# Kernel tuning notes

Hardware: AMD Instinct MI355X
Metric: run time of the kernel (lower is better)

The kernel has to match this reference:

```python
import jax, jax.numpy as jnp
import numpy as np

N_DRUG, D, K = 846, 64, 1024
N_REL, N_ENT = 200, 100000
BN_EPS = 1e-5

def setup_inputs() -> dict:
    key = jax.random.key(0)
    ks = jax.random.split(key, 10)
    return {
        "drug_table": jax.random.normal(ks[0], (N_DRUG, D), jnp.float32),
        "rela_table": jax.random.normal(ks[1], (N_REL, D), jnp.float32),
        "ent_table": jax.random.normal(ks[2], (N_ENT, D), jnp.float32),
        "W1": jax.random.normal(ks[3], (N_DRUG, D, D), jnp.float32),
        "b1": jax.random.normal(ks[4], (K, D), jnp.float32),
        "W2": jax.random.normal(ks[5], (N_DRUG, D, D), jnp.float32),
        "b2": jax.random.normal(ks[6], (K, D), jnp.float32),
        "lin_w": jax.random.normal(ks[7], (D, 2 * D), jnp.float32) * (6.0 / (3 * D)) ** 0.5,
        "lin_b": jnp.zeros((D,), jnp.float32),
        "bn_w": jnp.ones((D,), jnp.float32),
        "bn_b": jnp.zeros((D,), jnp.float32),
        "drug_name": jnp.arange(N_DRUG, dtype=jnp.int64 if jax.config.jax_enable_x64 else jnp.int32),
        "adj_tail": jax.random.randint(ks[8], (N_DRUG, K), 0, N_ENT),
        "adj_relation": jax.random.randint(ks[9], (N_DRUG, K), 0, N_REL),
    }

def reference(drug_table, rela_table, ent_table, W1, b1, W2, b2,
              lin_w, lin_b, bn_w, bn_b, drug_name, adj_tail, adj_relation):
    drug_emb = drug_table[drug_name]          # [N, D]
    rela_emb = rela_table[adj_relation]       # [N, K, D]
    ent_emb = ent_table[adj_tail]             # [N, K, D]
    # per-drug relation-modulated transform
    drug_rel = drug_emb[:, None, :] * rela_emb                     # [N, K, D]
    h = jax.nn.relu(jnp.einsum('nkd,nde->nke', drug_rel, W1) + b1)  # [N, K, D]
    h = jnp.einsum('nkd,nde->nke', h, W2) + b2                      # [N, K, D]
    score = jax.nn.softmax(jnp.sum(h, axis=-1), axis=1)             # [N, K]
    weighted_ent = jnp.einsum('nk,nkd->nd', score, ent_emb)         # [N, D]
    drug_e = jnp.concatenate([weighted_ent, drug_emb], axis=1)      # [N, 2D]
    y = jax.nn.relu(drug_e @ lin_w.T + lin_b)                       # [N, D]
    # BatchNorm1d in training mode: biased batch statistics
    mean = jnp.mean(y, axis=0)
    var = jnp.mean((y - mean) ** 2, axis=0)
    out = (y - mean) * jax.lax.rsqrt(var + BN_EPS) * bn_w + bn_b
    return out
```

## Files before the change

kernel.cpp:

```cpp
#include <hip/hip_runtime.h>


#define NDRUG 846
#define KNB   1024
#define NREL  200
#define BN_EPS 1e-5f

#define NW2   ((NDRUG*64 + 255)/256)
#define NRELT 13312
#define NRELB (NRELT/256)

typedef __attribute__((ext_vector_type(8))) short short8;
typedef __attribute__((ext_vector_type(4))) float f32x4;

__device__ __forceinline__ unsigned short f2bf(float x){
    unsigned u = __float_as_uint(x);
    unsigned r = u + 0x7fffu + ((u >> 16) & 1u);
    return (unsigned short)(r >> 16);
}
__device__ __forceinline__ float bf2f(unsigned short h){
    return __uint_as_float(((unsigned)h) << 16);
}

__global__ void prep_kernel(const float* __restrict__ b2, const float* __restrict__ W2,
                            const float* __restrict__ rela_table,
                            float* __restrict__ b2s, float* __restrict__ w2sum_g,
                            unsigned short* __restrict__ relah,
                            unsigned short* __restrict__ relal){
    int b = blockIdx.x;
    int t = threadIdx.x;
    if (b < 4){
        int k = b*256 + t;
        const float4* p = (const float4*)(b2 + (size_t)k*64);
        float s = 0.f;
        #pragma unroll
        for (int i = 0; i < 16; ++i){ float4 v = p[i]; s += v.x+v.y+v.z+v.w; }
        b2s[k] = s;
    } else if (b < 4 + NW2){
        int idx = (b - 4)*256 + t;
        if (idx < NDRUG*64){
            const float4* p = (const float4*)(W2 + (size_t)idx*64);
            float s = 0.f;
            #pragma unroll
            for (int i = 0; i < 16; ++i){ float4 v = p[i]; s += v.x+v.y+v.z+v.w; }
            w2sum_g[idx] = s;
        }
    } else {
        int idx = (b - 4 - NW2)*256 + t;
        int j  = idx & 7;
        int ln = (idx >> 3) & 63;
        int ss = (idx >> 9) & 1;
        int mt = idx >> 10;
        int r = mt*16 + (ln & 15); if (r > 199) r = 199;
        int d = ss*32 + ((ln >> 4) << 3) + j;
        float v = rela_table[r*64 + d];
        unsigned short h = (unsigned short)(__float_as_uint(v) >> 16);
        relah[idx] = h;
        relal[idx] = f2bf(v - bf2f(h));
    }
}

__global__ __launch_bounds__(512) void gnn_a4x(
    const float* __restrict__ drug_table, const unsigned short* __restrict__ relah,
    const unsigned short* __restrict__ relal,
    const float* __restrict__ W1,         const float* __restrict__ b1,
    const float* __restrict__ w2sum_g,    const int* __restrict__ drug_name,
    const int* __restrict__ adj_rel,
    float* __restrict__ scoresA,          float* __restrict__ scoresB)
{
    __shared__ __align__(16) float sS[6400];
    __shared__ __align__(16) float w2s[32];
    __shared__ float drug[64];
    unsigned short* Bh = (unsigned short*)sS;
    unsigned short* Bl = (unsigned short*)(sS + 1024);

    const int t = threadIdx.x;
    const int lane = t & 63;
    const int w = t >> 6;
    const int lg = lane >> 4;
    const int l15 = lane & 15;
    const int n = blockIdx.x;
    const int ehalf = blockIdx.y;
    const int e_base = ehalf << 5;

    if (t < 64) drug[t] = drug_table[(size_t)drug_name[n]*64 + t];
    if (t >= 64 && t < 96) w2s[t - 64] = w2sum_g[n*64 + e_base + (t - 64)];
    __syncthreads();

    {
        const float* W1n = W1 + (size_t)n*4096;
        #pragma unroll
        for (int p = 0; p < 4; ++p){
            int idx = p*512 + t;
            int d = idx >> 5, eo = idx & 31;
            float v = W1n[d*64 + e_base + eo] * drug[d];
            int ss = d >> 5, j = d & 7, lgb = (d >> 3) & 3, nn = eo >> 4;
            int ln = (lgb << 4) | (eo & 15);
            int dst = (((ss<<1)|nn)*64 + ln)*8 + j;
            unsigned short h = (unsigned short)(__float_as_uint(v) >> 16);
            Bh[dst] = h;
            Bl[dst] = f2bf(v - bf2f(h));
        }
    }
    __syncthreads();

    short8 bhr[4], blr[4];
    #pragma unroll
    for (int f = 0; f < 4; ++f){
        bhr[f] = *(const short8*)&Bh[(f*64 + lane)*8];
        blr[f] = *(const short8*)&Bl[(f*64 + lane)*8];
    }
    __syncthreads();

    const short8* Ah_t = (const short8*)relah;
    const short8* Al_t = (const short8*)relal;

    #pragma unroll 1
    for (int mi = 0; mi < 2; ++mi){
        int mt = w + 8*mi;
        if (mt < 13){
            short8 Ah0 = Ah_t[(mt*2+0)*64 + lane];
            short8 Ah1 = Ah_t[(mt*2+1)*64 + lane];
            short8 Al0 = Al_t[(mt*2+0)*64 + lane];
            short8 Al1 = Al_t[(mt*2+1)*64 + lane];
            f32x4 acc[2] = {};
            #pragma unroll
            for (int nn = 0; nn < 2; ++nn){
                acc[nn] = __builtin_amdgcn_mfma_f32_16x16x32_bf16(Ah0, bhr[nn],   acc[nn], 0,0,0);
                acc[nn] = __builtin_amdgcn_mfma_f32_16x16x32_bf16(Ah0, blr[nn],   acc[nn], 0,0,0);
                acc[nn] = __builtin_amdgcn_mfma_f32_16x16x32_bf16(Al0, bhr[nn],   acc[nn], 0,0,0);
                acc[nn] = __builtin_amdgcn_mfma_f32_16x16x32_bf16(Ah1, bhr[2+nn], acc[nn], 0,0,0);
                acc[nn] = __builtin_amdgcn_mfma_f32_16x16x32_bf16(Ah1, blr[2+nn], acc[nn], 0,0,0);
                acc[nn] = __builtin_amdgcn_mfma_f32_16x16x32_bf16(Al1, bhr[2+nn], acc[nn], 0,0,0);
            }
            int rb = mt*16 + (lg<<2);
            #pragma unroll
            for (int nn = 0; nn < 2; ++nn){
                int eo = (nn<<4) | l15;
                int slot = eo >> 2, wrd = eo & 3;
                #pragma unroll
                for (int q = 0; q < 4; ++q){
                    int r = rb + q;
                    if (r < 200)
                        sS[r*32 + ((slot ^ (r & 7))<<2) + wrd] = acc[nn][q];
                }
            }
        }
    }
    __syncthreads();

    const int* arel = adj_rel + (size_t)n*KNB;
    float* sout = (ehalf ? scoresB : scoresA) + (size_t)n*KNB;
    const int ec = lane & 3;
    f32x4 w2r[2];
    #pragma unroll
    for (int j = 0; j < 2; ++j) w2r[j] = *(const f32x4*)&w2s[ec*8 + j*4];

    int rr8[8];
    #pragma unroll
    for (int pass = 0; pass < 8; ++pass)
        rr8[pass] = arel[pass*128 + w*16 + (lane >> 2)];

    #pragma unroll 2
    for (int pass = 0; pass < 8; ++pass){
        int k = pass*128 + w*16 + (lane >> 2);
        int rr = rr8[pass];
        const float* b1p = b1 + (size_t)k*64 + e_base + ec*8;
        float sc = 0.f;
        #pragma unroll
        for (int j = 0; j < 2; ++j){
            int slot = ec*2 + j;
            f32x4 s4 = *(const f32x4*)&sS[rr*32 + ((slot ^ (rr & 7))<<2)];
            f32x4 bq = *(const f32x4*)(b1p + 4*j);
            #pragma unroll
            for (int q = 0; q < 4; ++q)
                sc += fmaxf(s4[q] + bq[q], 0.f) * w2r[j][q];
        }
        sc += __shfl_xor(sc, 1);
        sc += __shfl_xor(sc, 2);
        if (ec == 0) sout[k] = sc;
    }
}

__global__ __launch_bounds__(256,6) void softgather(
    const float* __restrict__ scoresA,  const float* __restrict__ scoresB,
    const float* __restrict__ b2s,
    const int* __restrict__ adj_tail,   const float* __restrict__ ent_table,
    const float* __restrict__ drug_table, const int* __restrict__ drug_name,
    const float* __restrict__ lin_w,    const float* __restrict__ lin_b,
    float* __restrict__ y_out)
{
    __shared__ float sE[KNB];
    __shared__ int list[KNB];
    __shared__ int segc[17];
    __shared__ float red[256];
    __shared__ float wepart[4][64];
    __shared__ float de[128];

    const int t = threadIdx.x;
    const int lane = t & 63;
    const int w = t >> 6;
    const int n = blockIdx.x;

    float dpre = 0.f;
    if (t < 64) dpre = drug_table[(size_t)drug_name[n]*64 + t];

    const float* sgA = scoresA + (size_t)n*KNB;
    const float* sgB = scoresB + (size_t)n*KNB;
    float sv[4]; float mx = -1e30f;
    #pragma unroll
    for (int i = 0; i < 4; ++i){
        int k = t + (i<<8);
        sv[i] = sgA[k] + sgB[k] + b2s[k];
        mx = fmaxf(mx, sv[i]);
    }
    #pragma unroll
    for (int off = 1; off < 64; off <<= 1) mx = fmaxf(mx, __shfl_xor(mx, off, 64));
    if (lane == 0) red[w] = mx;
    __syncthreads();
    mx = fmaxf(fmaxf(red[0], red[1]), fmaxf(red[2], red[3]));
    float ei[4]; float ps = 0.f;
    #pragma unroll
    for (int i = 0; i < 4; ++i){
        ei[i] = __expf(sv[i] - mx);
        sE[t + (i<<8)] = ei[i];
        ps += ei[i];
    }
    #pragma unroll
    for (int off = 1; off < 64; off <<= 1) ps += __shfl_xor(ps, off, 64);
    if (lane == 0) red[8 + w] = ps;
    __syncthreads();
    const float inv = 1.f / (red[8]+red[9]+red[10]+red[11]);

    unsigned long long bal[4]; int pos[4];
    #pragma unroll
    for (int i = 0; i < 4; ++i){
        bool nz = (ei[i] != 0.f);
        bal[i] = __ballot(nz);
        pos[i] = (int)__popcll(bal[i] & ((1ull << lane) - 1ull));
        if (lane == 0) segc[i*4 + w] = (int)__popcll(bal[i]);
    }
    __syncthreads();
    if (t == 0){
        int acc = 0;
        #pragma unroll
        for (int s = 0; s < 16; ++s){ int c = segc[s]; segc[s] = acc; acc += c; }
        segc[16] = acc;
    }
    __syncthreads();
    #pragma unroll
    for (int i = 0; i < 4; ++i){
        if (ei[i] != 0.f)
            list[segc[i*4 + w] + pos[i]] = (i<<8) + (w<<6) + lane;
    }
    const int C = segc[16];
    __syncthreads();

    const int* atail = adj_tail + (size_t)n*KNB;
    float awe = 0.f;
    {
        int j = w;
        float ev0 = 0.f, row0 = 0.f;
        if (j < C){
            int k0 = list[j];
            ev0 = sE[k0];
            row0 = ent_table[(size_t)atail[k0]*64 + lane];
        }
        while (j < C){
            int jn = j + 4;
            float ev1 = 0.f, row1 = 0.f;
            if (jn < C){
                int k1 = list[jn];
                ev1 = sE[k1];
                row1 = ent_table[(size_t)atail[k1]*64 + lane];
            }
            awe += ev0 * row0;
            ev0 = ev1; row0 = row1; j = jn;
        }
    }
    wepart[w][lane] = awe;
    __syncthreads();
    if (t < 64){
        de[t]    = (wepart[0][t]+wepart[1][t]+wepart[2][t]+wepart[3][t]) * inv;
        de[64+t] = dpre;
    }
    __syncthreads();

    float yp = 0.f;
    #pragma unroll
    for (int ii = 0; ii < 32; ++ii){
        int i = w*32 + ii;
        yp += de[i] * lin_w[lane*128 + i];
    }
    red[t] = yp;
    __syncthreads();
    if (t < 64){
        float yv = lin_b[t] + red[t] + red[64+t] + red[128+t] + red[192+t];
        y_out[(size_t)n*64 + t] = fmaxf(yv, 0.f);
    }
}

__global__ void bn_kernel(const float* __restrict__ y, const float* __restrict__ bn_w,
                          const float* __restrict__ bn_b, float* __restrict__ out){
    __shared__ float r1[4], r2[4];
    const int j = blockIdx.x;
    const int t = threadIdx.x;
    float s1 = 0.f, s2 = 0.f;
    for (int i = t; i < NDRUG; i += 256){
        float v = y[(size_t)i*64 + j];
        s1 += v; s2 += v*v;
    }
    #pragma unroll
    for (int off = 1; off < 64; off <<= 1){
        s1 += __shfl_xor(s1, off, 64);
        s2 += __shfl_xor(s2, off, 64);
    }
    int w = t >> 6, lane = t & 63;
    if (lane == 0){ r1[w] = s1; r2[w] = s2; }
    __syncthreads();
    s1 = r1[0]+r1[1]+r1[2]+r1[3];
    s2 = r2[0]+r2[1]+r2[2]+r2[3];
    float mean = s1 * (1.f/NDRUG);
    float var  = s2 * (1.f/NDRUG) - mean*mean;
    float sc = rsqrtf(var + BN_EPS) * bn_w[j];
    float sh = bn_b[j] - mean*sc;
    for (int i = t; i < NDRUG; i += 256)
        out[(size_t)i*64 + j] = y[(size_t)i*64 + j]*sc + sh;
}

extern "C" void kernel_launch(void* const* d_in, const int* in_sizes, int n_in,
                              void* d_out, int out_size, void* d_ws, size_t ws_size,
                              hipStream_t stream) {
    const float* drug_table = (const float*)d_in[0];
    const float* rela_table = (const float*)d_in[1];
    const float* ent_table  = (const float*)d_in[2];
    const float* W1    = (const float*)d_in[3];
    const float* b1    = (const float*)d_in[4];
    const float* W2    = (const float*)d_in[5];
    const float* b2    = (const float*)d_in[6];
    const float* lin_w = (const float*)d_in[7];
    const float* lin_b = (const float*)d_in[8];
    const float* bn_w  = (const float*)d_in[9];
    const float* bn_b  = (const float*)d_in[10];
    const int* drug_name = (const int*)d_in[11];
    const int* adj_tail  = (const int*)d_in[12];
    const int* adj_rel   = (const int*)d_in[13];
    float* out = (float*)d_out;

    float* b2s     = (float*)d_ws;
    float* yb      = b2s + KNB;
    float* w2sumg  = yb + NDRUG*64;
    float* scoresA = w2sumg + NDRUG*64;
    float* scoresB = scoresA + (size_t)NDRUG*KNB;
    unsigned short* relah = (unsigned short*)(scoresB + (size_t)NDRUG*KNB);
    unsigned short* relal = relah + NRELT;

    prep_kernel<<<4 + NW2 + NRELB, 256, 0, stream>>>(
        b2, W2, rela_table, b2s, w2sumg, relah, relal);
    gnn_a4x<<<dim3(NDRUG,2), 512, 0, stream>>>(drug_table, relah, relal, W1, b1,
                                               w2sumg, drug_name, adj_rel,
                                               scoresA, scoresB);
    softgather<<<NDRUG, 256, 0, stream>>>(scoresA, scoresB, b2s, adj_tail, ent_table,
                                          drug_table, drug_name, lin_w, lin_b, yb);
    bn_kernel<<<64, 256, 0, stream>>>(yb, bn_w, bn_b, out);
}
```

Baseline: 47.29 us.

## Precompute drug-scaled split-bf16 W1 fragments in prep kernel

Moves the drug-scaled W1 conversion into bf16 hi/lo MFMA-fragment layout out of the main scoring kernel and into the prep kernel, which now writes it to workspace. The scoring kernel loads B fragments straight from global memory, dropping its shared-memory staging and two block barriers. W1 is read once per drug instead of once per e-half, but this adds a global write and re-read of the converted fragments and a larger, LDS-heavy prep kernel.

```diff
diff --git a/kernel.cpp b/kernel.cpp
--- a/kernel.cpp
+++ b/kernel.cpp
@@ -9,6 +9,7 @@
 #define NW2   ((NDRUG*64 + 255)/256)
 #define NRELT 13312
 #define NRELB (NRELT/256)
+#define PREPW1 (4 + NW2 + NRELB)
 
 typedef __attribute__((ext_vector_type(8))) short short8;
 typedef __attribute__((ext_vector_type(4))) float f32x4;
@@ -24,9 +25,16 @@
 
 __global__ void prep_kernel(const float* __restrict__ b2, const float* __restrict__ W2,
                             const float* __restrict__ rela_table,
+                            const float* __restrict__ drug_table,
+                            const float* __restrict__ W1,
+                            const int* __restrict__ drug_name,
                             float* __restrict__ b2s, float* __restrict__ w2sum_g,
                             unsigned short* __restrict__ relah,
-                            unsigned short* __restrict__ relal){
+                            unsigned short* __restrict__ relal,
+                            unsigned short* __restrict__ w1h,
+                            unsigned short* __restrict__ w1l){
+    __shared__ float drugs[64];
+    __shared__ unsigned short BhL[4096], BlL[4096];
     int b = blockIdx.x;
     int t = threadIdx.x;
     if (b < 4){
@@ -45,7 +53,7 @@
             for (int i = 0; i < 16; ++i){ float4 v = p[i]; s += v.x+v.y+v.z+v.w; }
             w2sum_g[idx] = s;
         }
-    } else {
+    } else if (b < PREPW1){
         int idx = (b - 4 - NW2)*256 + t;
         int j  = idx & 7;
         int ln = (idx >> 3) & 63;
@@ -57,22 +65,46 @@
         unsigned short h = (unsigned short)(__float_as_uint(v) >> 16);
         relah[idx] = h;
         relal[idx] = f2bf(v - bf2f(h));
-    }
-}
-
-__global__ __launch_bounds__(512) void gnn_a4x(
-    const float* __restrict__ drug_table, const unsigned short* __restrict__ relah,
-    const unsigned short* __restrict__ relal,
-    const float* __restrict__ W1,         const float* __restrict__ b1,
-    const float* __restrict__ w2sum_g,    const int* __restrict__ drug_name,
+    } else {
+        int n = b - PREPW1;
+        if (t < 64) drugs[t] = drug_table[(size_t)drug_name[n]*64 + t];
+        __syncthreads();
+        const float* W1n = W1 + (size_t)n*4096;
+        #pragma unroll
+        for (int p = 0; p < 16; ++p){
+            int idx = p*256 + t;
+            int d = idx >> 6, e = idx & 63;
+            float v = W1n[idx] * drugs[d];
+            int ss = d >> 5, j = d & 7, lgb = (d >> 3) & 3;
+            int f = ss*4 + (e >> 4);
+            int ln = (lgb << 4) | (e & 15);
+            int dst = (f*64 + ln)*8 + j;
+            unsigned short h = (unsigned short)(__float_as_uint(v) >> 16);
+            BhL[dst] = h;
+            BlL[dst] = f2bf(v - bf2f(h));
+        }
+        __syncthreads();
+        short8* outh = (short8*)w1h + (size_t)n*512;
+        short8* outl = (short8*)w1l + (size_t)n*512;
+        const short8* inh = (const short8*)BhL;
+        const short8* inl = (const short8*)BlL;
+        #pragma unroll
+        for (int it = 0; it < 2; ++it){
+            outh[it*256 + t] = inh[it*256 + t];
+            outl[it*256 + t] = inl[it*256 + t];
+        }
+    }
+}
+
+__global__ __launch_bounds__(512) void gnn_b(
+    const unsigned short* __restrict__ relah, const unsigned short* __restrict__ relal,
+    const unsigned short* __restrict__ w1h,   const unsigned short* __restrict__ w1l,
+    const float* __restrict__ b1,             const float* __restrict__ w2sum_g,
     const int* __restrict__ adj_rel,
-    float* __restrict__ scoresA,          float* __restrict__ scoresB)
+    float* __restrict__ scoresA,              float* __restrict__ scoresB)
 {
     __shared__ __align__(16) float sS[6400];
     __shared__ __align__(16) float w2s[32];
-    __shared__ float drug[64];
-    unsigned short* Bh = (unsigned short*)sS;
-    unsigned short* Bl = (unsigned short*)(sS + 1024);
 
     const int t = threadIdx.x;
     const int lane = t & 63;
@@ -83,34 +115,19 @@
     const int ehalf = blockIdx.y;
     const int e_base = ehalf << 5;
 
-    if (t < 64) drug[t] = drug_table[(size_t)drug_name[n]*64 + t];
-    if (t >= 64 && t < 96) w2s[t - 64] = w2sum_g[n*64 + e_base + (t - 64)];
-    __syncthreads();
-
-    {
-        const float* W1n = W1 + (size_t)n*4096;
-        #pragma unroll
-        for (int p = 0; p < 4; ++p){
-            int idx = p*512 + t;
-            int d = idx >> 5, eo = idx & 31;
-            float v = W1n[d*64 + e_base + eo] * drug[d];
-            int ss = d >> 5, j = d & 7, lgb = (d >> 3) & 3, nn = eo >> 4;
-            int ln = (lgb << 4) | (eo & 15);
-            int dst = (((ss<<1)|nn)*64 + ln)*8 + j;
-            unsigned short h = (unsigned short)(__float_as_uint(v) >> 16);
-            Bh[dst] = h;
-            Bl[dst] = f2bf(v - bf2f(h));
-        }
-    }
-    __syncthreads();
-
+    if (t < 32) w2s[t] = w2sum_g[n*64 + e_base + t];
+
+    const short8* bht = (const short8*)w1h + (size_t)n*512;
+    const short8* blt = (const short8*)w1l + (size_t)n*512;
     short8 bhr[4], blr[4];
     #pragma unroll
-    for (int f = 0; f < 4; ++f){
-        bhr[f] = *(const short8*)&Bh[(f*64 + lane)*8];
-        blr[f] = *(const short8*)&Bl[(f*64 + lane)*8];
-    }
-    __syncthreads();
+    for (int ss = 0; ss < 2; ++ss)
+        #pragma unroll
+        for (int nn = 0; nn < 2; ++nn){
+            int f = ss*4 + ehalf*2 + nn;
+            bhr[ss*2+nn] = bht[f*64 + lane];
+            blr[ss*2+nn] = blt[f*64 + lane];
+        }
 
     const short8* Ah_t = (const short8*)relah;
     const short8* Al_t = (const short8*)relal;
@@ -354,12 +371,14 @@
     float* scoresB = scoresA + (size_t)NDRUG*KNB;
     unsigned short* relah = (unsigned short*)(scoresB + (size_t)NDRUG*KNB);
     unsigned short* relal = relah + NRELT;
-
-    prep_kernel<<<4 + NW2 + NRELB, 256, 0, stream>>>(
-        b2, W2, rela_table, b2s, w2sumg, relah, relal);
-    gnn_a4x<<<dim3(NDRUG,2), 512, 0, stream>>>(drug_table, relah, relal, W1, b1,
-                                               w2sumg, drug_name, adj_rel,
-                                               scoresA, scoresB);
+    unsigned short* w1h   = relal + NRELT;
+    unsigned short* w1l   = w1h + (size_t)NDRUG*4096;
+
+    prep_kernel<<<PREPW1 + NDRUG, 256, 0, stream>>>(
+        b2, W2, rela_table, drug_table, W1, drug_name,
+        b2s, w2sumg, relah, relal, w1h, w1l);
+    gnn_b<<<dim3(NDRUG,2), 512, 0, stream>>>(relah, relal, w1h, w1l, b1,
+                                             w2sumg, adj_rel, scoresA, scoresB);
     softgather<<<NDRUG, 256, 0, stream>>>(scoresA, scoresB, b2s, adj_tail, ent_table,
                                           drug_table, drug_name, lin_w, lin_b, yb);
     bn_kernel<<<64, 256, 0, stream>>>(yb, bn_w, bn_b, out);
```

Result: slower. 51.10 us (+8.1%).

## Fuse score kernel and softmax-gather kernel into one per-drug block

Applied to the files above, without the earlier changes.

Merges the two-half score computation and the softmax/gather/linear kernel into a single 512-thread block per drug. Each block now loops over both 32-column halves itself, keeping the scores in shared memory instead of writing them to global and reading them back. This removes the global score round-trip and one kernel launch. In exchange the grid shrinks from 2x846 blocks to 846, with more shared memory per block, which reduces parallelism and occupancy.

```diff
diff --git a/kernel.cpp b/kernel.cpp
--- a/kernel.cpp
+++ b/kernel.cpp
@@ -60,19 +60,29 @@
     }
 }
 
-__global__ __launch_bounds__(512) void gnn_a4x(
+__global__ __launch_bounds__(512) void fused_drug(
     const float* __restrict__ drug_table, const unsigned short* __restrict__ relah,
     const unsigned short* __restrict__ relal,
     const float* __restrict__ W1,         const float* __restrict__ b1,
-    const float* __restrict__ w2sum_g,    const int* __restrict__ drug_name,
-    const int* __restrict__ adj_rel,
-    float* __restrict__ scoresA,          float* __restrict__ scoresB)
+    const float* __restrict__ w2sum_g,    const float* __restrict__ b2s,
+    const int* __restrict__ drug_name,    const int* __restrict__ adj_rel,
+    const int* __restrict__ adj_tail,     const float* __restrict__ ent_table,
+    const float* __restrict__ lin_w,      const float* __restrict__ lin_b,
+    float* __restrict__ y_out)
 {
     __shared__ __align__(16) float sS[6400];
-    __shared__ __align__(16) float w2s[32];
+    __shared__ __align__(16) unsigned short Bbuf[8192];
+    __shared__ __align__(16) float w2s[64];
     __shared__ float drug[64];
-    unsigned short* Bh = (unsigned short*)sS;
-    unsigned short* Bl = (unsigned short*)(sS + 1024);
+    __shared__ float red[512];
+    __shared__ int   segc[17];
+    __shared__ float wepart[8][64];
+    __shared__ float de[128];
+
+    unsigned short* Bh = Bbuf;
+    unsigned short* Bl = Bbuf + 4096;
+    float* sE  = (float*)Bbuf;
+    int*  list = (int*)(Bbuf + 2048);
 
     const int t = threadIdx.x;
     const int lane = t & 63;
@@ -80,15 +90,27 @@
     const int lg = lane >> 4;
     const int l15 = lane & 15;
     const int n = blockIdx.x;
-    const int ehalf = blockIdx.y;
-    const int e_base = ehalf << 5;
 
     if (t < 64) drug[t] = drug_table[(size_t)drug_name[n]*64 + t];
-    if (t >= 64 && t < 96) w2s[t - 64] = w2sum_g[n*64 + e_base + (t - 64)];
-    __syncthreads();
-
-    {
-        const float* W1n = W1 + (size_t)n*4096;
+    else if (t < 128) w2s[t - 64] = w2sum_g[n*64 + (t - 64)];
+    __syncthreads();
+
+    const int* arel = adj_rel + (size_t)n*KNB;
+    int rr8[8];
+    #pragma unroll
+    for (int pass = 0; pass < 8; ++pass)
+        rr8[pass] = arel[pass*128 + w*16 + (lane >> 2)];
+
+    const short8* Ah_t = (const short8*)relah;
+    const short8* Al_t = (const short8*)relal;
+    const float* W1n = W1 + (size_t)n*4096;
+    const int ec = lane & 3;
+    float sc8[8] = {0.f,0.f,0.f,0.f,0.f,0.f,0.f,0.f};
+
+    #pragma unroll 1
+    for (int eh = 0; eh < 2; ++eh){
+        const int e_base = eh << 5;
+
         #pragma unroll
         for (int p = 0; p < 4; ++p){
             int idx = p*512 + t;
@@ -101,144 +123,121 @@
             Bh[dst] = h;
             Bl[dst] = f2bf(v - bf2f(h));
         }
-    }
-    __syncthreads();
-
-    short8 bhr[4], blr[4];
-    #pragma unroll
-    for (int f = 0; f < 4; ++f){
-        bhr[f] = *(const short8*)&Bh[(f*64 + lane)*8];
-        blr[f] = *(const short8*)&Bl[(f*64 + lane)*8];
-    }
-    __syncthreads();
-
-    const short8* Ah_t = (const short8*)relah;
-    const short8* Al_t = (const short8*)relal;
-
-    #pragma unroll 1
-    for (int mi = 0; mi < 2; ++mi){
-        int mt = w + 8*mi;
-        if (mt < 13){
-            short8 Ah0 = Ah_t[(mt*2+0)*64 + lane];
-            short8 Ah1 = Ah_t[(mt*2+1)*64 + lane];
-            short8 Al0 = Al_t[(mt*2+0)*64 + lane];
-            short8 Al1 = Al_t[(mt*2+1)*64 + lane];
-            f32x4 acc[2] = {};
-            #pragma unroll
-            for (int nn = 0; nn < 2; ++nn){
-                acc[nn] = __builtin_amdgcn_mfma_f32_16x16x32_bf16(Ah0, bhr[nn],   acc[nn], 0,0,0);
-                acc[nn] = __builtin_amdgcn_mfma_f32_16x16x32_bf16(Ah0, blr[nn],   acc[nn], 0,0,0);
-                acc[nn] = __builtin_amdgcn_mfma_f32_16x16x32_bf16(Al0, bhr[nn],   acc[nn], 0,0,0);
-                acc[nn] = __builtin_amdgcn_mfma_f32_16x16x32_bf16(Ah1, bhr[2+nn], acc[nn], 0,0,0);
-                acc[nn] = __builtin_amdgcn_mfma_f32_16x16x32_bf16(Ah1, blr[2+nn], acc[nn], 0,0,0);
-                acc[nn] = __builtin_amdgcn_mfma_f32_16x16x32_bf16(Al1, bhr[2+nn], acc[nn], 0,0,0);
-            }
-            int rb = mt*16 + (lg<<2);
-            #pragma unroll
-            for (int nn = 0; nn < 2; ++nn){
-                int eo = (nn<<4) | l15;
-                int slot = eo >> 2, wrd = eo & 3;
+        __syncthreads();
+
+        short8 bhr[4], blr[4];
+        #pragma unroll
+        for (int f = 0; f < 4; ++f){
+            bhr[f] = *(const short8*)&Bh[(f*64 + lane)*8];
+            blr[f] = *(const short8*)&Bl[(f*64 + lane)*8];
+        }
+
+        #pragma unroll 1
+        for (int mi = 0; mi < 2; ++mi){
+            int mt = w + 8*mi;
+            if (mt < 13){
+                short8 Ah0 = Ah_t[(mt*2+0)*64 + lane];
+                short8 Ah1 = Ah_t[(mt*2+1)*64 + lane];
+                short8 Al0 = Al_t[(mt*2+0)*64 + lane];
+                short8 Al1 = Al_t[(mt*2+1)*64 + lane];
+                f32x4 acc[2] = {};
                 #pragma unroll
-                for (int q = 0; q < 4; ++q){
-                    int r = rb + q;
-                    if (r < 200)
-                        sS[r*32 + ((slot ^ (r & 7))<<2) + wrd] = acc[nn][q];
+                for (int nn = 0; nn < 2; ++nn){
+                    acc[nn] = __builtin_amdgcn_mfma_f32_16x16x32_bf16(Ah0, bhr[nn],   acc[nn], 0,0,0);
+                    acc[nn] = __builtin_amdgcn_mfma_f32_16x16x32_bf16(Ah0, blr[nn],   acc[nn], 0,0,0);
+                    acc[nn] = __builtin_amdgcn_mfma_f32_16x16x32_bf16(Al0, bhr[nn],   acc[nn], 0,0,0);
+                    acc[nn] = __builtin_amdgcn_mfma_f32_16x16x32_bf16(Ah1, bhr[2+nn], acc[nn], 0,0,0);
+                    acc[nn] = __builtin_amdgcn_mfma_f32_16x16x32_bf16(Ah1, blr[2+nn], acc[nn], 0,0,0);
+                    acc[nn] = __builtin_amdgcn_mfma_f32_16x16x32_bf16(Al1, bhr[2+nn], acc[nn], 0,0,0);
+                }
+                int rb = mt*16 + (lg<<2);
+                #pragma unroll
+                for (int nn = 0; nn < 2; ++nn){
+                    int eo = (nn<<4) | l15;
+                    int slot = eo >> 2, wrd = eo & 3;
+                    #pragma unroll
+                    for (int q = 0; q < 4; ++q){
+                        int r = rb + q;
+                        if (r < 200)
+                            sS[r*32 + ((slot ^ (r & 7))<<2) + wrd] = acc[nn][q];
+                    }
                 }
             }
         }
-    }
-    __syncthreads();
-
-    const int* arel = adj_rel + (size_t)n*KNB;
-    float* sout = (ehalf ? scoresB : scoresA) + (size_t)n*KNB;
-    const int ec = lane & 3;
-    f32x4 w2r[2];
-    #pragma unroll
-    for (int j = 0; j < 2; ++j) w2r[j] = *(const f32x4*)&w2s[ec*8 + j*4];
-
-    int rr8[8];
-    #pragma unroll
-    for (int pass = 0; pass < 8; ++pass)
-        rr8[pass] = arel[pass*128 + w*16 + (lane >> 2)];
-
-    #pragma unroll 2
+        __syncthreads();
+
+        f32x4 w2r[2];
+        #pragma unroll
+        for (int j = 0; j < 2; ++j) w2r[j] = *(const f32x4*)&w2s[e_base + ec*8 + j*4];
+
+        #pragma unroll 2
+        for (int pass = 0; pass < 8; ++pass){
+            int k = pass*128 + w*16 + (lane >> 2);
+            int rr = rr8[pass];
+            const float* b1p = b1 + (size_t)k*64 + e_base + ec*8;
+            float sc = 0.f;
+            #pragma unroll
+            for (int j = 0; j < 2; ++j){
+                int slot = ec*2 + j;
+                f32x4 s4 = *(const f32x4*)&sS[rr*32 + ((slot ^ (rr & 7))<<2)];
+                f32x4 bq = *(const f32x4*)(b1p + 4*j);
+                #pragma unroll
+                for (int q = 0; q < 4; ++q)
+                    sc += fmaxf(s4[q] + bq[q], 0.f) * w2r[j][q];
+            }
+            sc8[pass] += sc;
+        }
+        __syncthreads();
+    }
+
+    #pragma unroll
     for (int pass = 0; pass < 8; ++pass){
-        int k = pass*128 + w*16 + (lane >> 2);
-        int rr = rr8[pass];
-        const float* b1p = b1 + (size_t)k*64 + e_base + ec*8;
-        float sc = 0.f;
-        #pragma unroll
-        for (int j = 0; j < 2; ++j){
-            int slot = ec*2 + j;
-            f32x4 s4 = *(const f32x4*)&sS[rr*32 + ((slot ^ (rr & 7))<<2)];
-            f32x4 bq = *(const f32x4*)(b1p + 4*j);
-            #pragma unroll
-            for (int q = 0; q < 4; ++q)
-                sc += fmaxf(s4[q] + bq[q], 0.f) * w2r[j][q];
-        }
+        float sc = sc8[pass];
         sc += __shfl_xor(sc, 1);
         sc += __shfl_xor(sc, 2);
-        if (ec == 0) sout[k] = sc;
-    }
-}
-
-__global__ __launch_bounds__(256,6) void softgather(
-    const float* __restrict__ scoresA,  const float* __restrict__ scoresB,
-    const float* __restrict__ b2s,
-    const int* __restrict__ adj_tail,   const float* __restrict__ ent_table,
-    const float* __restrict__ drug_table, const int* __restrict__ drug_name,
-    const float* __restrict__ lin_w,    const float* __restrict__ lin_b,
-    float* __restrict__ y_out)
-{
-    __shared__ float sE[KNB];
-    __shared__ int list[KNB];
-    __shared__ int segc[17];
-    __shared__ float red[256];
-    __shared__ float wepart[4][64];
-    __shared__ float de[128];
-
-    const int t = threadIdx.x;
-    const int lane = t & 63;
-    const int w = t >> 6;
-    const int n = blockIdx.x;
-
-    float dpre = 0.f;
-    if (t < 64) dpre = drug_table[(size_t)drug_name[n]*64 + t];
-
-    const float* sgA = scoresA + (size_t)n*KNB;
-    const float* sgB = scoresB + (size_t)n*KNB;
-    float sv[4]; float mx = -1e30f;
-    #pragma unroll
-    for (int i = 0; i < 4; ++i){
-        int k = t + (i<<8);
-        sv[i] = sgA[k] + sgB[k] + b2s[k];
+        int k = pass*128 + w*16 + (lane >> 2);
+        if (ec == 0) sE[k] = sc + b2s[k];
+    }
+    __syncthreads();
+
+    float sv[2]; float mx = -1e30f;
+    #pragma unroll
+    for (int i = 0; i < 2; ++i){
+        sv[i] = sE[t + (i<<9)];
         mx = fmaxf(mx, sv[i]);
     }
     #pragma unroll
     for (int off = 1; off < 64; off <<= 1) mx = fmaxf(mx, __shfl_xor(mx, off, 64));
     if (lane == 0) red[w] = mx;
     __syncthreads();
-    mx = fmaxf(fmaxf(red[0], red[1]), fmaxf(red[2], red[3]));
-    float ei[4]; float ps = 0.f;
-    #pragma unroll
-    for (int i = 0; i < 4; ++i){
+    mx = red[0];
+    #pragma unroll
+    for (int s = 1; s < 8; ++s) mx = fmaxf(mx, red[s]);
+    float ei[2]; float ps = 0.f;
+    #pragma unroll
+    for (int i = 0; i < 2; ++i){
         ei[i] = __expf(sv[i] - mx);
-        sE[t + (i<<8)] = ei[i];
         ps += ei[i];
     }
+    __syncthreads();
+    #pragma unroll
+    for (int i = 0; i < 2; ++i) sE[t + (i<<9)] = ei[i];
     #pragma unroll
     for (int off = 1; off < 64; off <<= 1) ps += __shfl_xor(ps, off, 64);
-    if (lane == 0) red[8 + w] = ps;
-    __syncthreads();
-    const float inv = 1.f / (red[8]+red[9]+red[10]+red[11]);
-
-    unsigned long long bal[4]; int pos[4];
-    #pragma unroll
-    for (int i = 0; i < 4; ++i){
+    if (lane == 0) red[16 + w] = ps;
+    __syncthreads();
+    float pst = 0.f;
+    #pragma unroll
+    for (int s = 0; s < 8; ++s) pst += red[16 + s];
+    const float inv = 1.f / pst;
+
+    unsigned long long bal[2]; int pos[2];
+    #pragma unroll
+    for (int i = 0; i < 2; ++i){
         bool nz = (ei[i] != 0.f);
         bal[i] = __ballot(nz);
         pos[i] = (int)__popcll(bal[i] & ((1ull << lane) - 1ull));
-        if (lane == 0) segc[i*4 + w] = (int)__popcll(bal[i]);
+        if (lane == 0) segc[i*8 + w] = (int)__popcll(bal[i]);
     }
     __syncthreads();
     if (t == 0){
@@ -249,9 +248,9 @@
     }
     __syncthreads();
     #pragma unroll
-    for (int i = 0; i < 4; ++i){
+    for (int i = 0; i < 2; ++i){
         if (ei[i] != 0.f)
-            list[segc[i*4 + w] + pos[i]] = (i<<8) + (w<<6) + lane;
+            list[segc[i*8 + w] + pos[i]] = (i<<9) + (w<<6) + lane;
     }
     const int C = segc[16];
     __syncthreads();
@@ -267,7 +266,7 @@
             row0 = ent_table[(size_t)atail[k0]*64 + lane];
         }
         while (j < C){
-            int jn = j + 4;
+            int jn = j + 8;
             float ev1 = 0.f, row1 = 0.f;
             if (jn < C){
                 int k1 = list[jn];
@@ -281,21 +280,26 @@
     wepart[w][lane] = awe;
     __syncthreads();
     if (t < 64){
-        de[t]    = (wepart[0][t]+wepart[1][t]+wepart[2][t]+wepart[3][t]) * inv;
-        de[64+t] = dpre;
+        float s = 0.f;
+        #pragma unroll
+        for (int q = 0; q < 8; ++q) s += wepart[q][t];
+        de[t]    = s * inv;
+        de[64+t] = drug[t];
     }
     __syncthreads();
 
     float yp = 0.f;
     #pragma unroll
-    for (int ii = 0; ii < 32; ++ii){
-        int i = w*32 + ii;
+    for (int ii = 0; ii < 16; ++ii){
+        int i = w*16 + ii;
         yp += de[i] * lin_w[lane*128 + i];
     }
     red[t] = yp;
     __syncthreads();
     if (t < 64){
-        float yv = lin_b[t] + red[t] + red[64+t] + red[128+t] + red[192+t];
+        float yv = lin_b[t];
+        #pragma unroll
+        for (int q = 0; q < 8; ++q) yv += red[q*64 + t];
         y_out[(size_t)n*64 + t] = fmaxf(yv, 0.f);
     }
 }
@@ -350,17 +354,13 @@
     float* b2s     = (float*)d_ws;
     float* yb      = b2s + KNB;
     float* w2sumg  = yb + NDRUG*64;
-    float* scoresA = w2sumg + NDRUG*64;
-    float* scoresB = scoresA + (size_t)NDRUG*KNB;
-    unsigned short* relah = (unsigned short*)(scoresB + (size_t)NDRUG*KNB);
+    unsigned short* relah = (unsigned short*)(w2sumg + NDRUG*64);
     unsigned short* relal = relah + NRELT;
 
     prep_kernel<<<4 + NW2 + NRELB, 256, 0, stream>>>(
         b2, W2, rela_table, b2s, w2sumg, relah, relal);
-    gnn_a4x<<<dim3(NDRUG,2), 512, 0, stream>>>(drug_table, relah, relal, W1, b1,
-                                               w2sumg, drug_name, adj_rel,
-                                               scoresA, scoresB);
-    softgather<<<NDRUG, 256, 0, stream>>>(scoresA, scoresB, b2s, adj_tail, ent_table,
-                                          drug_table, drug_name, lin_w, lin_b, yb);
+    fused_drug<<<NDRUG, 512, 0, stream>>>(drug_table, relah, relal, W1, b1,
+                                          w2sumg, b2s, drug_name, adj_rel,
+                                          adj_tail, ent_table, lin_w, lin_b, yb);
     bn_kernel<<<64, 256, 0, stream>>>(yb, bn_w, bn_b, out);
 }
```

New measurement: 50.42 us. 6.6% more time.

## Split GNN score kernel into four output-column quarters with smaller blocks

Applied to the files above, without the earlier changes.

The score kernel now splits the 64 output columns into four 16-wide quarters instead of two halves, launching 846x4 blocks of 256 threads rather than 846x2 blocks of 512. The shared score table shrinks and drops the XOR swizzle for a padded stride-20 layout, and the adjacency index preload moves ahead of the MFMA phase. The softgather kernel sums four partial score buffers instead of two. The aim is more, smaller blocks for occupancy and latency hiding, at the cost of recomputing the relation-table MFMA and W1 staging per quarter and doubling partial-score traffic.

```diff
diff --git a/kernel.cpp b/kernel.cpp
--- a/kernel.cpp
+++ b/kernel.cpp
@@ -60,19 +60,18 @@
     }
 }
 
-__global__ __launch_bounds__(512) void gnn_a4x(
+__global__ __launch_bounds__(256) void gnn_q(
     const float* __restrict__ drug_table, const unsigned short* __restrict__ relah,
     const unsigned short* __restrict__ relal,
     const float* __restrict__ W1,         const float* __restrict__ b1,
     const float* __restrict__ w2sum_g,    const int* __restrict__ drug_name,
-    const int* __restrict__ adj_rel,
-    float* __restrict__ scoresA,          float* __restrict__ scoresB)
+    const int* __restrict__ adj_rel,      float* __restrict__ qpart)
 {
-    __shared__ __align__(16) float sS[6400];
-    __shared__ __align__(16) float w2s[32];
+    __shared__ __align__(16) float sS[4000];
+    __shared__ float w2s[16];
     __shared__ float drug[64];
     unsigned short* Bh = (unsigned short*)sS;
-    unsigned short* Bl = (unsigned short*)(sS + 1024);
+    unsigned short* Bl = (unsigned short*)sS + 1024;
 
     const int t = threadIdx.x;
     const int lane = t & 63;
@@ -80,23 +79,23 @@
     const int lg = lane >> 4;
     const int l15 = lane & 15;
     const int n = blockIdx.x;
-    const int ehalf = blockIdx.y;
-    const int e_base = ehalf << 5;
+    const int eq = blockIdx.y;
+    const int e_base = eq << 4;
 
     if (t < 64) drug[t] = drug_table[(size_t)drug_name[n]*64 + t];
-    if (t >= 64 && t < 96) w2s[t - 64] = w2sum_g[n*64 + e_base + (t - 64)];
+    else if (t < 80) w2s[t - 64] = w2sum_g[n*64 + e_base + (t - 64)];
     __syncthreads();
 
     {
         const float* W1n = W1 + (size_t)n*4096;
         #pragma unroll
         for (int p = 0; p < 4; ++p){
-            int idx = p*512 + t;
-            int d = idx >> 5, eo = idx & 31;
+            int idx = p*256 + t;
+            int d = idx >> 4, eo = idx & 15;
             float v = W1n[d*64 + e_base + eo] * drug[d];
-            int ss = d >> 5, j = d & 7, lgb = (d >> 3) & 3, nn = eo >> 4;
-            int ln = (lgb << 4) | (eo & 15);
-            int dst = (((ss<<1)|nn)*64 + ln)*8 + j;
+            int ss = d >> 5, j = d & 7, lgb = (d >> 3) & 3;
+            int ln = (lgb << 4) | eo;
+            int dst = (ss*64 + ln)*8 + j;
             unsigned short h = (unsigned short)(__float_as_uint(v) >> 16);
             Bh[dst] = h;
             Bl[dst] = f2bf(v - bf2f(h));
@@ -104,87 +103,75 @@
     }
     __syncthreads();
 
-    short8 bhr[4], blr[4];
-    #pragma unroll
-    for (int f = 0; f < 4; ++f){
+    short8 bhr[2], blr[2];
+    #pragma unroll
+    for (int f = 0; f < 2; ++f){
         bhr[f] = *(const short8*)&Bh[(f*64 + lane)*8];
         blr[f] = *(const short8*)&Bl[(f*64 + lane)*8];
     }
     __syncthreads();
 
+    const int* arel = adj_rel + (size_t)n*KNB;
+    int rr8[8];
+    #pragma unroll
+    for (int pass = 0; pass < 8; ++pass)
+        rr8[pass] = arel[pass*128 + w*32 + (lane >> 1)];
+
     const short8* Ah_t = (const short8*)relah;
     const short8* Al_t = (const short8*)relal;
 
     #pragma unroll 1
-    for (int mi = 0; mi < 2; ++mi){
-        int mt = w + 8*mi;
+    for (int mi = 0; mi < 4; ++mi){
+        int mt = w + 4*mi;
         if (mt < 13){
             short8 Ah0 = Ah_t[(mt*2+0)*64 + lane];
             short8 Ah1 = Ah_t[(mt*2+1)*64 + lane];
             short8 Al0 = Al_t[(mt*2+0)*64 + lane];
             short8 Al1 = Al_t[(mt*2+1)*64 + lane];
-            f32x4 acc[2] = {};
-            #pragma unroll
-            for (int nn = 0; nn < 2; ++nn){
-                acc[nn] = __builtin_amdgcn_mfma_f32_16x16x32_bf16(Ah0, bhr[nn],   acc[nn], 0,0,0);
-                acc[nn] = __builtin_amdgcn_mfma_f32_16x16x32_bf16(Ah0, blr[nn],   acc[nn], 0,0,0);
-                acc[nn] = __builtin_amdgcn_mfma_f32_16x16x32_bf16(Al0, bhr[nn],   acc[nn], 0,0,0);
-                acc[nn] = __builtin_amdgcn_mfma_f32_16x16x32_bf16(Ah1, bhr[2+nn], acc[nn], 0,0,0);
-                acc[nn] = __builtin_amdgcn_mfma_f32_16x16x32_bf16(Ah1, blr[2+nn], acc[nn], 0,0,0);
-                acc[nn] = __builtin_amdgcn_mfma_f32_16x16x32_bf16(Al1, bhr[2+nn], acc[nn], 0,0,0);
-            }
+            f32x4 acc = {0.f,0.f,0.f,0.f};
+            acc = __builtin_amdgcn_mfma_f32_16x16x32_bf16(Ah0, bhr[0], acc, 0,0,0);
+            acc = __builtin_amdgcn_mfma_f32_16x16x32_bf16(Ah0, blr[0], acc, 0,0,0);
+            acc = __builtin_amdgcn_mfma_f32_16x16x32_bf16(Al0, bhr[0], acc, 0,0,0);
+            acc = __builtin_amdgcn_mfma_f32_16x16x32_bf16(Ah1, bhr[1], acc, 0,0,0);
+            acc = __builtin_amdgcn_mfma_f32_16x16x32_bf16(Ah1, blr[1], acc, 0,0,0);
+            acc = __builtin_amdgcn_mfma_f32_16x16x32_bf16(Al1, bhr[1], acc, 0,0,0);
             int rb = mt*16 + (lg<<2);
             #pragma unroll
-            for (int nn = 0; nn < 2; ++nn){
-                int eo = (nn<<4) | l15;
-                int slot = eo >> 2, wrd = eo & 3;
-                #pragma unroll
-                for (int q = 0; q < 4; ++q){
-                    int r = rb + q;
-                    if (r < 200)
-                        sS[r*32 + ((slot ^ (r & 7))<<2) + wrd] = acc[nn][q];
-                }
+            for (int q = 0; q < 4; ++q){
+                int r = rb + q;
+                if (r < 200) sS[r*20 + l15] = acc[q];
             }
         }
     }
     __syncthreads();
 
-    const int* arel = adj_rel + (size_t)n*KNB;
-    float* sout = (ehalf ? scoresB : scoresA) + (size_t)n*KNB;
-    const int ec = lane & 3;
+    const int ec = lane & 1;
     f32x4 w2r[2];
     #pragma unroll
     for (int j = 0; j < 2; ++j) w2r[j] = *(const f32x4*)&w2s[ec*8 + j*4];
-
-    int rr8[8];
-    #pragma unroll
-    for (int pass = 0; pass < 8; ++pass)
-        rr8[pass] = arel[pass*128 + w*16 + (lane >> 2)];
+    float* qp = qpart + ((size_t)eq*NDRUG + n)*KNB;
 
     #pragma unroll 2
     for (int pass = 0; pass < 8; ++pass){
-        int k = pass*128 + w*16 + (lane >> 2);
+        int k = pass*128 + w*32 + (lane >> 1);
         int rr = rr8[pass];
         const float* b1p = b1 + (size_t)k*64 + e_base + ec*8;
         float sc = 0.f;
         #pragma unroll
         for (int j = 0; j < 2; ++j){
-            int slot = ec*2 + j;
-            f32x4 s4 = *(const f32x4*)&sS[rr*32 + ((slot ^ (rr & 7))<<2)];
+            f32x4 s4 = *(const f32x4*)&sS[rr*20 + ec*8 + j*4];
             f32x4 bq = *(const f32x4*)(b1p + 4*j);
             #pragma unroll
             for (int q = 0; q < 4; ++q)
                 sc += fmaxf(s4[q] + bq[q], 0.f) * w2r[j][q];
         }
         sc += __shfl_xor(sc, 1);
-        sc += __shfl_xor(sc, 2);
-        if (ec == 0) sout[k] = sc;
+        if (ec == 0) qp[k] = sc;
     }
 }
 
 __global__ __launch_bounds__(256,6) void softgather(
-    const float* __restrict__ scoresA,  const float* __restrict__ scoresB,
-    const float* __restrict__ b2s,
+    const float* __restrict__ qpart,    const float* __restrict__ b2s,
     const int* __restrict__ adj_tail,   const float* __restrict__ ent_table,
     const float* __restrict__ drug_table, const int* __restrict__ drug_name,
     const float* __restrict__ lin_w,    const float* __restrict__ lin_b,
@@ -205,13 +192,15 @@
     float dpre = 0.f;
     if (t < 64) dpre = drug_table[(size_t)drug_name[n]*64 + t];
 
-    const float* sgA = scoresA + (size_t)n*KNB;
-    const float* sgB = scoresB + (size_t)n*KNB;
+    const float* q0 = qpart + (size_t)n*KNB;
+    const float* q1 = q0 + (size_t)NDRUG*KNB;
+    const float* q2 = q1 + (size_t)NDRUG*KNB;
+    const float* q3 = q2 + (size_t)NDRUG*KNB;
     float sv[4]; float mx = -1e30f;
     #pragma unroll
     for (int i = 0; i < 4; ++i){
         int k = t + (i<<8);
-        sv[i] = sgA[k] + sgB[k] + b2s[k];
+        sv[i] = ((q0[k] + q1[k]) + (q2[k] + q3[k])) + b2s[k];
         mx = fmaxf(mx, sv[i]);
     }
     #pragma unroll
@@ -350,17 +339,15 @@
     float* b2s     = (float*)d_ws;
     float* yb      = b2s + KNB;
     float* w2sumg  = yb + NDRUG*64;
-    float* scoresA = w2sumg + NDRUG*64;
-    float* scoresB = scoresA + (size_t)NDRUG*KNB;
-    unsigned short* relah = (unsigned short*)(scoresB + (size_t)NDRUG*KNB);
+    unsigned short* relah = (unsigned short*)(w2sumg + NDRUG*64);
     unsigned short* relal = relah + NRELT;
+    float* qpart   = (float*)(relal + NRELT);
 
     prep_kernel<<<4 + NW2 + NRELB, 256, 0, stream>>>(
         b2, W2, rela_table, b2s, w2sumg, relah, relal);
-    gnn_a4x<<<dim3(NDRUG,2), 512, 0, stream>>>(drug_table, relah, relal, W1, b1,
-                                               w2sumg, drug_name, adj_rel,
-                                               scoresA, scoresB);
-    softgather<<<NDRUG, 256, 0, stream>>>(scoresA, scoresB, b2s, adj_tail, ent_table,
+    gnn_q<<<dim3(NDRUG,4), 256, 0, stream>>>(drug_table, relah, relal, W1, b1,
+                                             w2sumg, drug_name, adj_rel, qpart);
+    softgather<<<NDRUG, 256, 0, stream>>>(qpart, b2s, adj_tail, ent_table,
                                           drug_table, drug_name, lin_w, lin_b, yb);
     bn_kernel<<<64, 256, 0, stream>>>(yb, bn_w, bn_b, out);
 }
```

New measurement: 55.64 us. 1.18x slower.
